# Kernel optimization log

Hardware: AMD Instinct MI355X
Metric: run time of the kernel (lower is better)

## Reference

```python
import jax, jax.numpy as jnp
import numpy as np
import math

NUM_HEADS = 16
KEY_DIM = 64
MODEL_DIM = 1024
NEG_INF = -1000000000.0


def _get_slopes(n):
    def pow2_slopes(n):
        start = 2 ** (-2 ** (-(math.log2(n) - 3)))
        return [start * start ** i for i in range(n)]
    if math.log2(n).is_integer():
        s = pow2_slopes(n)
    else:
        c = 2 ** math.floor(math.log2(n))
        s = pow2_slopes(c) + pow2_slopes(2 * c)[0::2][: n - c]
    return jnp.asarray(s, dtype=jnp.float32)


def setup_inputs() -> dict:
    key = jax.random.key(0)
    ks = jax.random.split(key, 11)
    B, S, D = 4, 2048, MODEL_DIM
    P = NUM_HEADS * KEY_DIM
    sd = 1.0 / math.sqrt(D)
    return {
        "query": jax.random.normal(ks[0], (B, S, D), jnp.float32),
        "key": jax.random.normal(ks[1], (B, S, D), jnp.float32),
        "value": jax.random.normal(ks[2], (B, S, D), jnp.float32),
        "Wq": jax.random.normal(ks[3], (D, P), jnp.float32) * sd,
        "bq": jnp.zeros((P,), jnp.float32),
        "Wk": jax.random.normal(ks[4], (D, P), jnp.float32) * sd,
        "bk": jnp.zeros((P,), jnp.float32),
        "Wv": jax.random.normal(ks[5], (D, P), jnp.float32) * sd,
        "bv": jnp.zeros((P,), jnp.float32),
        "Wo": jax.random.normal(ks[6], (P, D), jnp.float32) * (1.0 / math.sqrt(P)),
        "bo": jnp.zeros((D,), jnp.float32),
    }


def reference(query, key, value, Wq, bq, Wk, bk, Wv, bv, Wo, bo):
    B, S, _ = query.shape
    H, Kd = NUM_HEADS, KEY_DIM

    def split_heads(x):  # [B,S,H*Kd] -> [B,H,S,Kd]
        return x.reshape(B, S, H, Kd).transpose(0, 2, 1, 3)

    q = split_heads(query @ Wq + bq)
    k = split_heads(key @ Wk + bk)
    v = split_heads(value @ Wv + bv)

    logits = jnp.einsum("bhqd,bhkd->bhqk", q, k) / jnp.sqrt(jnp.float32(Kd))

    i = jnp.arange(S)[:, None]
    j = jnp.arange(S)[None, :]
    causal = jnp.where(i >= j, 0.0, NEG_INF).astype(jnp.float32)  # [S,S]
    rel = (i - j).astype(jnp.float32)  # [S,S]
    slopes = _get_slopes(H)  # [H]
    alibi = slopes[:, None, None] * rel  # [H,S,S]
    logits = logits + causal[None, None, :, :] + alibi[None, :, :, :]

    weights = jax.nn.softmax(logits, axis=-1)
    attn = jnp.einsum("bhqk,bhkd->bhqd", weights, v)
    concat = attn.transpose(0, 2, 1, 3).reshape(B, S, H * Kd)
    return concat @ Wo + bo
```

## Files before the change

### kernel.cpp

```cpp
#include <hip/hip_runtime.h>

#define B_ 4
#define S_ 2048
#define D_ 1024
#define H_ 16
#define KD_ 64
#define P_ 1024
#define M_ (B_*S_)

typedef unsigned short u16;
typedef unsigned int u32;
typedef __attribute__((ext_vector_type(4))) float f32x4;
typedef __attribute__((ext_vector_type(8))) __bf16 bf16x8;

__device__ __forceinline__ u16 f2bf(float f) {
  u32 x = __float_as_uint(f);
  return (u16)((x + 0x7fffu + ((x >> 16) & 1u)) >> 16);
}

__device__ __forceinline__ void gl_lds16(const u16* g, u16* l) {
  __builtin_amdgcn_global_load_lds((__attribute__((address_space(1))) void*)g,
                                   (__attribute__((address_space(3))) void*)l, 16, 0, 0);
}

__device__ __forceinline__ u32 pkbf(float a, float b) {
  return __builtin_amdgcn_perm(__float_as_uint(b) + 0x8000u,
                               __float_as_uint(a) + 0x8000u, 0x07060302u);
}

__global__ void cvt3_kernel(const float* __restrict__ q, const float* __restrict__ k,
                            const float* __restrict__ v,
                            u16* __restrict__ Xq, u16* __restrict__ Xk, u16* __restrict__ Xv) {
  const int z = blockIdx.y;
  const float* in = z == 0 ? q : z == 1 ? k : v;
  u16* out = z == 0 ? Xq : z == 1 ? Xk : Xv;
  int i = blockIdx.x * 256 + threadIdx.x;
  float4 vv = ((const float4*)in)[i];
  ((u32*)out)[i*2+0] = (u32)f2bf(vv.x) | ((u32)f2bf(vv.y) << 16);
  ((u32*)out)[i*2+1] = (u32)f2bf(vv.z) | ((u32)f2bf(vv.w) << 16);
}

__global__ void transpose_cvt4(const float* __restrict__ Wq, const float* __restrict__ Wk,
                               const float* __restrict__ Wv, const float* __restrict__ Wo,
                               u16* __restrict__ WqT, u16* __restrict__ WkT,
                               u16* __restrict__ WvT, u16* __restrict__ WoT) {
  const int z = blockIdx.z;
  const float* in = z == 0 ? Wq : z == 1 ? Wk : z == 2 ? Wv : Wo;
  u16* out = z == 0 ? WqT : z == 1 ? WkT : z == 2 ? WvT : WoT;
  __shared__ float tile[32][33];
  int bx = blockIdx.x * 32, by = blockIdx.y * 32;
  int tx = threadIdx.x, ty = threadIdx.y;
  #pragma unroll
  for (int kk = 0; kk < 4; ++kk)
    tile[ty + kk*8][tx] = in[(by + ty + kk*8) * 1024 + bx + tx];
  __syncthreads();
  #pragma unroll
  for (int kk = 0; kk < 4; ++kk)
    out[(bx + ty + kk*8) * 1024 + by + tx] = f2bf(tile[tx][ty + kk*8]);
}

__global__ __launch_bounds__(256) void gemm_qkv(
    const u16* __restrict__ Xq, const u16* __restrict__ Xk, const u16* __restrict__ Xv,
    const u16* __restrict__ WqT, const u16* __restrict__ WkT, const u16* __restrict__ WvT,
    const float* __restrict__ bq, const float* __restrict__ bk, const float* __restrict__ bv,
    u16* __restrict__ Qb, u16* __restrict__ Kb, u16* __restrict__ Vt)
{
  constexpr int K = 1024, N = 1024, BK = 32;
  const int z = blockIdx.z;
  const u16* A  = z == 0 ? Xq  : z == 1 ? Xk  : Xv;
  const u16* Bt = z == 0 ? WqT : z == 1 ? WkT : WvT;
  const float* bias = z == 0 ? bq : z == 1 ? bk : bv;

  __shared__ alignas(16) u16 As[128*BK];
  __shared__ alignas(16) u16 Bs[128*BK];
  const int tid = threadIdx.x;
  const int w = tid >> 6, l = tid & 63;
  const int quad = l >> 4, l16 = l & 15;
  const int wm = (w >> 1) * 64, wn = (w & 1) * 64;
  const long mBase = (long)blockIdx.x * 128;
  const int  nBase = blockIdx.y * 128;

  f32x4 acc[4][4] = {};
  const int off0 = w*1024 + l*16;

  for (int kb = 0; kb < K/BK; ++kb) {
    __syncthreads();
    #pragma unroll
    for (int p = 0; p < 2; ++p) {
      int off = p*4096 + off0;
      int row = off >> 6;
      int cb  = off & 63;
      const u16* ga = A  + (mBase + row)*K + kb*BK + (cb >> 1);
      const u16* gb = Bt + ((long)(nBase + row))*K + kb*BK + (cb >> 1);
      gl_lds16(ga, (u16*)((char*)As + p*4096 + w*1024));
      gl_lds16(gb, (u16*)((char*)Bs + p*4096 + w*1024));
    }
    __syncthreads();
    bf16x8 af[4], bf[4];
    #pragma unroll
    for (int i = 0; i < 4; ++i) af[i] = *(const bf16x8*)&As[(wm + i*16 + l16)*BK + quad*8];
    #pragma unroll
    for (int j = 0; j < 4; ++j) bf[j] = *(const bf16x8*)&Bs[(wn + j*16 + l16)*BK + quad*8];
    #pragma unroll
    for (int i = 0; i < 4; ++i)
      #pragma unroll
      for (int j = 0; j < 4; ++j)
        acc[i][j] = __builtin_amdgcn_mfma_f32_16x16x32_bf16(af[i], bf[j], acc[i][j], 0, 0, 0);
  }

  if (z < 2) {
    u16* Cout = z == 0 ? Qb : Kb;
    #pragma unroll
    for (int i = 0; i < 4; ++i)
      #pragma unroll
      for (int j = 0; j < 4; ++j)
        #pragma unroll
        for (int r = 0; r < 4; ++r) {
          long row = mBase + wm + i*16 + quad*4 + r;
          int  col = nBase + wn + j*16 + l16;
          Cout[row*N + col] = f2bf(acc[i][j][r] + bias[col]);
        }
  } else {
    #pragma unroll
    for (int i = 0; i < 4; ++i)
      #pragma unroll
      for (int j = 0; j < 4; ++j) {
        int  col  = nBase + wn + j*16 + l16;
        long row0 = mBase + wm + i*16 + quad*4;
        int  bb = (int)(row0 >> 11);
        int  ss = (int)(row0 & 2047);
        float bcol = bias[col];
        float v0 = acc[i][j][0] + bcol, v1 = acc[i][j][1] + bcol;
        float v2 = acc[i][j][2] + bcol, v3 = acc[i][j][3] + bcol;
        uint2 pk;
        pk.x = (u32)f2bf(v0) | ((u32)f2bf(v1) << 16);
        pk.y = (u32)f2bf(v2) | ((u32)f2bf(v3) << 16);
        *(uint2*)&Vt[((long)(bb*16) * 64 + col) * 2048 + ss] = pk;
      }
  }
}

__global__ __launch_bounds__(256) void gemm_out(const u16* __restrict__ A,
                                                const u16* __restrict__ Bt,
                                                const float* __restrict__ bias,
                                                float* __restrict__ Cout)
{
  constexpr int K = 1024, N = 1024, BK = 32;
  __shared__ alignas(16) u16 As[128*BK];
  __shared__ alignas(16) u16 Bs[128*BK];
  const int tid = threadIdx.x;
  const int w = tid >> 6, l = tid & 63;
  const int quad = l >> 4, l16 = l & 15;
  const int wm = (w >> 1) * 64, wn = (w & 1) * 64;
  const long mBase = (long)blockIdx.x * 128;
  const int  nBase = blockIdx.y * 128;

  f32x4 acc[4][4] = {};
  const int off0 = w*1024 + l*16;

  for (int kb = 0; kb < K/BK; ++kb) {
    __syncthreads();
    #pragma unroll
    for (int p = 0; p < 2; ++p) {
      int off = p*4096 + off0;
      int row = off >> 6;
      int cb  = off & 63;
      const u16* ga = A  + (mBase + row)*K + kb*BK + (cb >> 1);
      const u16* gb = Bt + ((long)(nBase + row))*K + kb*BK + (cb >> 1);
      gl_lds16(ga, (u16*)((char*)As + p*4096 + w*1024));
      gl_lds16(gb, (u16*)((char*)Bs + p*4096 + w*1024));
    }
    __syncthreads();
    bf16x8 af[4], bf[4];
    #pragma unroll
    for (int i = 0; i < 4; ++i) af[i] = *(const bf16x8*)&As[(wm + i*16 + l16)*BK + quad*8];
    #pragma unroll
    for (int j = 0; j < 4; ++j) bf[j] = *(const bf16x8*)&Bs[(wn + j*16 + l16)*BK + quad*8];
    #pragma unroll
    for (int i = 0; i < 4; ++i)
      #pragma unroll
      for (int j = 0; j < 4; ++j)
        acc[i][j] = __builtin_amdgcn_mfma_f32_16x16x32_bf16(af[i], bf[j], acc[i][j], 0, 0, 0);
  }

  #pragma unroll
  for (int i = 0; i < 4; ++i)
    #pragma unroll
    for (int j = 0; j < 4; ++j)
      #pragma unroll
      for (int r = 0; r < 4; ++r) {
        long row = mBase + wm + i*16 + quad*4 + r;
        int  col = nBase + wn + j*16 + l16;
        Cout[row*N + col] = acc[i][j][r] + bias[col];
      }
}

#define PST 136
__global__ __launch_bounds__(64, 3) void attn_kernel(const u16* __restrict__ Qb,
                                                     const u16* __restrict__ Kb,
                                                     const u16* __restrict__ Vt,
                                                     u16* __restrict__ Ob)
{
  const int n = blockIdx.x;
  const int qt = 15 - (n >> 8);
  const int r8 = n & 255;
  const int b = r8 >> 6, h = (r8 >> 2) & 15, w = r8 & 3;
  const int l = threadIdx.x;
  const int quad = l >> 4, l16 = l & 15;
  const float LOG2E = 1.44269504089f;
  const float slope = exp2f(-0.5f * (float)(h + 1));
  const float c1  = 0.125f * LOG2E;
  const float sl2 = slope * LOG2E;

  __shared__ alignas(16) u16 Ps[2][16][PST];

  const int q0 = qt*128 + w*32;
  const u16* Qp = Qb + ((long)(b*S_ + q0))*P_ + h*KD_;
  const u16* Kp = Kb + ((long)(b*S_))*P_ + h*KD_;
  const u16* Vp = Vt + ((long)(b*H_ + h))*KD_*S_;

  bf16x8 qf[2][2];
  #pragma unroll
  for (int i = 0; i < 2; ++i)
    #pragma unroll
    for (int kk = 0; kk < 2; ++kk)
      qf[i][kk] = *(const bf16x8*)&Qp[(long)(i*16 + l16)*P_ + kk*32 + quad*8];

  f32x4 o[2][4] = {};
  float lsum[2] = {0.f, 0.f};
  const float rs1 = sl2, rs2 = 2.f*sl2, rs3 = 3.f*sl2;

  for (int kt = 0; kt < qt; ++kt) {
    const u16* kts = Kp + (long)(kt*128 + l16)*P_;
    #pragma unroll
    for (int jh = 0; jh < 2; ++jh) {
      f32x4 st[2][4];
      #pragma unroll
      for (int jj = 0; jj < 4; ++jj) {
        const int j = jh*4 + jj;
        const u16* kp = kts + (long)(j*16)*P_;
        bf16x8 kf0 = *(const bf16x8*)(kp + quad*8);
        bf16x8 kf1 = *(const bf16x8*)(kp + 32 + quad*8);
        #pragma unroll
        for (int i = 0; i < 2; ++i) {
          f32x4 t = {};
          t = __builtin_amdgcn_mfma_f32_16x16x32_bf16(kf0, qf[i][0], t, 0, 0, 0);
          t = __builtin_amdgcn_mfma_f32_16x16x32_bf16(kf1, qf[i][1], t, 0, 0, 0);
          st[i][jj] = t;
        }
      }
      #pragma unroll
      for (int i = 0; i < 2; ++i)
        #pragma unroll
        for (int jj = 0; jj < 4; ++jj) {
          const int j = jh*4 + jj;
          const float kb  = (float)(kt*128 + j*16 + quad*4);
          const float bij = -sl2 * kb;
          float p0 = __builtin_amdgcn_exp2f(fmaf(st[i][jj][0], c1, bij));
          float p1 = __builtin_amdgcn_exp2f(fmaf(st[i][jj][1], c1, bij) - rs1);
          float p2 = __builtin_amdgcn_exp2f(fmaf(st[i][jj][2], c1, bij) - rs2);
          float p3 = __builtin_amdgcn_exp2f(fmaf(st[i][jj][3], c1, bij) - rs3);
          lsum[i] += (p0 + p1) + (p2 + p3);
          uint2 pk; pk.x = pkbf(p0, p1); pk.y = pkbf(p2, p3);
          *(uint2*)&Ps[i][l16][j*16 + quad*4] = pk;
        }
    }
    #pragma unroll
    for (int ks = 0; ks < 4; ++ks) {
      bf16x8 pb0 = *(const bf16x8*)&Ps[0][l16][ks*32 + quad*8];
      bf16x8 pb1 = *(const bf16x8*)&Ps[1][l16][ks*32 + quad*8];
      #pragma unroll
      for (int jn = 0; jn < 4; ++jn) {
        bf16x8 vf = *(const bf16x8*)&Vp[(long)(jn*16 + l16)*S_ + kt*128 + ks*32 + quad*8];
        o[0][jn] = __builtin_amdgcn_mfma_f32_16x16x32_bf16(vf, pb0, o[0][jn], 0, 0, 0);
        o[1][jn] = __builtin_amdgcn_mfma_f32_16x16x32_bf16(vf, pb1, o[1][jn], 0, 0, 0);
      }
    }
  }

  {
    const int kt = qt;
    const int jmax = 2*w + 2, ksmax = w + 1;
    const u16* kts = Kp + (long)(kt*128 + l16)*P_;
    for (int j = 0; j < jmax; ++j) {
      const u16* kp = kts + (long)(j*16)*P_;
      bf16x8 kf0 = *(const bf16x8*)(kp + quad*8);
      bf16x8 kf1 = *(const bf16x8*)(kp + 32 + quad*8);
      const int kl0 = j*16 + quad*4;
      const float kb  = (float)(kt*128 + kl0);
      #pragma unroll
      for (int i = 0; i < 2; ++i) {
        f32x4 t = {};
        t = __builtin_amdgcn_mfma_f32_16x16x32_bf16(kf0, qf[i][0], t, 0, 0, 0);
        t = __builtin_amdgcn_mfma_f32_16x16x32_bf16(kf1, qf[i][1], t, 0, 0, 0);
        const int ql = w*32 + i*16 + l16;
        const float bij = -sl2 * kb;
        float x0 = fmaf(t[0], c1, bij);
        float x1 = fmaf(t[1], c1, bij) - rs1;
        float x2 = fmaf(t[2], c1, bij) - rs2;
        float x3 = fmaf(t[3], c1, bij) - rs3;
        if (kl0 + 0 > ql) x0 = -1e30f;
        if (kl0 + 1 > ql) x1 = -1e30f;
        if (kl0 + 2 > ql) x2 = -1e30f;
        if (kl0 + 3 > ql) x3 = -1e30f;
        float p0 = __builtin_amdgcn_exp2f(x0);
        float p1 = __builtin_amdgcn_exp2f(x1);
        float p2 = __builtin_amdgcn_exp2f(x2);
        float p3 = __builtin_amdgcn_exp2f(x3);
        lsum[i] += (p0 + p1) + (p2 + p3);
        uint2 pk; pk.x = pkbf(p0, p1); pk.y = pkbf(p2, p3);
        *(uint2*)&Ps[i][l16][j*16 + quad*4] = pk;
      }
    }
    for (int ks = 0; ks < ksmax; ++ks) {
      bf16x8 pb0 = *(const bf16x8*)&Ps[0][l16][ks*32 + quad*8];
      bf16x8 pb1 = *(const bf16x8*)&Ps[1][l16][ks*32 + quad*8];
      #pragma unroll
      for (int jn = 0; jn < 4; ++jn) {
        bf16x8 vf = *(const bf16x8*)&Vp[(long)(jn*16 + l16)*S_ + kt*128 + ks*32 + quad*8];
        o[0][jn] = __builtin_amdgcn_mfma_f32_16x16x32_bf16(vf, pb0, o[0][jn], 0, 0, 0);
        o[1][jn] = __builtin_amdgcn_mfma_f32_16x16x32_bf16(vf, pb1, o[1][jn], 0, 0, 0);
      }
    }
  }

  #pragma unroll
  for (int i = 0; i < 2; ++i) {
    lsum[i] += __shfl_xor(lsum[i], 16, 64);
    lsum[i] += __shfl_xor(lsum[i], 32, 64);
    const float inv = 1.0f / lsum[i];
    #pragma unroll
    for (int jn = 0; jn < 4; ++jn) {
      float v0 = o[i][jn][0] * inv, v1 = o[i][jn][1] * inv;
      float v2 = o[i][jn][2] * inv, v3 = o[i][jn][3] * inv;
      uint2 pk;
      pk.x = (u32)f2bf(v0) | ((u32)f2bf(v1) << 16);
      pk.y = (u32)f2bf(v2) | ((u32)f2bf(v3) << 16);
      *(uint2*)&Ob[((long)(b*S_ + q0 + i*16 + l16))*P_ + h*KD_ + jn*16 + quad*4] = pk;
    }
  }
}

extern "C" void kernel_launch(void* const* d_in, const int* in_sizes, int n_in,
                              void* d_out, int out_size, void* d_ws, size_t ws_size,
                              hipStream_t stream) {
  const float* q  = (const float*)d_in[0];
  const float* k  = (const float*)d_in[1];
  const float* v  = (const float*)d_in[2];
  const float* Wq = (const float*)d_in[3];
  const float* bq = (const float*)d_in[4];
  const float* Wk = (const float*)d_in[5];
  const float* bk = (const float*)d_in[6];
  const float* Wv = (const float*)d_in[7];
  const float* bv = (const float*)d_in[8];
  const float* Wo = (const float*)d_in[9];
  const float* bo = (const float*)d_in[10];

  const size_t X_ELEMS = (size_t)M_ * P_;
  const size_t W_ELEMS = (size_t)D_ * P_;
  u16* ws  = (u16*)d_ws;
  u16* Xq  = ws;
  u16* Xk  = Xq  + X_ELEMS;
  u16* Xv  = Xk  + X_ELEMS;
  u16* WqT = Xv  + X_ELEMS;
  u16* WkT = WqT + W_ELEMS;
  u16* WvT = WkT + W_ELEMS;
  u16* WoT = WvT + W_ELEMS;
  u16* Qb  = WoT + W_ELEMS;
  u16* Kb  = Qb  + X_ELEMS;
  u16* Vt  = Kb  + X_ELEMS;
  u16* Attn = Xq;

  cvt3_kernel<<<dim3((unsigned)(X_ELEMS/4/256), 3), 256, 0, stream>>>(q, k, v, Xq, Xk, Xv);

  transpose_cvt4<<<dim3(32, 32, 4), dim3(32, 8), 0, stream>>>(Wq, Wk, Wv, Wo,
                                                              WqT, WkT, WvT, WoT);

  gemm_qkv<<<dim3(M_/128, P_/128, 3), 256, 0, stream>>>(Xq, Xk, Xv, WqT, WkT, WvT,
                                                        bq, bk, bv, Qb, Kb, Vt);

  attn_kernel<<<dim3(4096), 64, 0, stream>>>(Qb, Kb, Vt, Attn);

  gemm_out<<<dim3(M_/128, P_/128), 256, 0, stream>>>(Attn, WoT, bo, (float*)d_out);
}
```

Measured before the change: 402.8 us.

## Keep attention probabilities in registers via permlane swaps instead of LDS

The attention kernel now gives each wave 16 query rows instead of 32 and launches 256-thread blocks of four waves. The softmax probability tiles are no longer staged through shared memory. They are rearranged into the MFMA B-operand layout in registers using permlane32/16 swaps, with a ds_bpermute fallback. This removes the LDS round trip and cuts register pressure, allowing more waves per CU. The cost is that each K and V fragment is loaded by twice as many waves, which doubles global and L2 traffic per query row.

```diff
diff --git a/kernel.cpp b/kernel.cpp
--- a/kernel.cpp
+++ b/kernel.cpp
@@ -10,6 +10,7 @@
 
 typedef unsigned short u16;
 typedef unsigned int u32;
+typedef __attribute__((ext_vector_type(2))) unsigned u32x2;
 typedef __attribute__((ext_vector_type(4))) float f32x4;
 typedef __attribute__((ext_vector_type(8))) __bf16 bf16x8;
 
@@ -27,6 +28,28 @@
   return __builtin_amdgcn_perm(__float_as_uint(b) + 0x8000u,
                                __float_as_uint(a) + 0x8000u, 0x07060302u);
 }
+
+#if __has_builtin(__builtin_amdgcn_permlane32_swap) && __has_builtin(__builtin_amdgcn_permlane16_swap)
+__device__ __forceinline__ void plswap(u32& a, u32& b) {
+  u32x2 r32 = __builtin_amdgcn_permlane32_swap(a, b, false, false);
+  u32x2 r16 = __builtin_amdgcn_permlane16_swap(r32[0], r32[1], false, false);
+  a = r16[0]; b = r16[1];
+}
+#else
+__device__ __forceinline__ void plswap(u32& a, u32& b) {
+  const int l = threadIdx.x & 63;
+  const int quad = l >> 4, l16 = l & 15;
+  int i0 = (((quad & 1) * 32) + l16) * 4;
+  int i1 = i0 + 64;
+  int a_lo = __builtin_amdgcn_ds_bpermute(i0, (int)a);
+  int b_lo = __builtin_amdgcn_ds_bpermute(i0, (int)b);
+  int a_hi = __builtin_amdgcn_ds_bpermute(i1, (int)a);
+  int b_hi = __builtin_amdgcn_ds_bpermute(i1, (int)b);
+  u32 na = (quad < 2) ? (u32)a_lo : (u32)b_lo;
+  u32 nb = (quad < 2) ? (u32)a_hi : (u32)b_hi;
+  a = na; b = nb;
+}
+#endif
 
 __global__ void cvt3_kernel(const float* __restrict__ q, const float* __restrict__ k,
                             const float* __restrict__ v,
@@ -195,149 +218,142 @@
       }
 }
 
-#define PST 136
-__global__ __launch_bounds__(64, 3) void attn_kernel(const u16* __restrict__ Qb,
-                                                     const u16* __restrict__ Kb,
-                                                     const u16* __restrict__ Vt,
-                                                     u16* __restrict__ Ob)
+__global__ __launch_bounds__(256, 8) void attn_kernel(const u16* __restrict__ Qb,
+                                                      const u16* __restrict__ Kb,
+                                                      const u16* __restrict__ Vt,
+                                                      u16* __restrict__ Ob)
 {
   const int n = blockIdx.x;
-  const int qt = 15 - (n >> 8);
-  const int r8 = n & 255;
-  const int b = r8 >> 6, h = (r8 >> 2) & 15, w = r8 & 3;
-  const int l = threadIdx.x;
+  const int qt = 15 - (n >> 7);
+  const int r7 = n & 127;
+  const int bh = r7 >> 1;
+  const int b = bh >> 4, h = bh & 15;
+  const int sw = (r7 & 1) * 4 + (threadIdx.x >> 6);
+  const int l = threadIdx.x & 63;
   const int quad = l >> 4, l16 = l & 15;
   const float LOG2E = 1.44269504089f;
   const float slope = exp2f(-0.5f * (float)(h + 1));
   const float c1  = 0.125f * LOG2E;
   const float sl2 = slope * LOG2E;
-
-  __shared__ alignas(16) u16 Ps[2][16][PST];
-
-  const int q0 = qt*128 + w*32;
+  const float rs1 = sl2, rs2 = 2.f*sl2, rs3 = 3.f*sl2;
+
+  const int q0 = qt*128 + sw*16;
   const u16* Qp = Qb + ((long)(b*S_ + q0))*P_ + h*KD_;
   const u16* Kp = Kb + ((long)(b*S_))*P_ + h*KD_;
   const u16* Vp = Vt + ((long)(b*H_ + h))*KD_*S_;
 
-  bf16x8 qf[2][2];
+  bf16x8 qf[2];
   #pragma unroll
-  for (int i = 0; i < 2; ++i)
-    #pragma unroll
-    for (int kk = 0; kk < 2; ++kk)
-      qf[i][kk] = *(const bf16x8*)&Qp[(long)(i*16 + l16)*P_ + kk*32 + quad*8];
-
-  f32x4 o[2][4] = {};
-  float lsum[2] = {0.f, 0.f};
-  const float rs1 = sl2, rs2 = 2.f*sl2, rs3 = 3.f*sl2;
+  for (int kk = 0; kk < 2; ++kk)
+    qf[kk] = *(const bf16x8*)&Qp[(long)l16*P_ + kk*32 + quad*8];
+
+  f32x4 o[4] = {};
+  float lsum = 0.f;
 
   for (int kt = 0; kt < qt; ++kt) {
     const u16* kts = Kp + (long)(kt*128 + l16)*P_;
-    #pragma unroll
-    for (int jh = 0; jh < 2; ++jh) {
-      f32x4 st[2][4];
-      #pragma unroll
-      for (int jj = 0; jj < 4; ++jj) {
-        const int j = jh*4 + jj;
+    const float kbase = (float)(kt*128);
+    #pragma unroll
+    for (int ks = 0; ks < 4; ++ks) {
+      u32 pw[2][2];
+      #pragma unroll
+      for (int jp = 0; jp < 2; ++jp) {
+        const int j = 2*ks + jp;
         const u16* kp = kts + (long)(j*16)*P_;
         bf16x8 kf0 = *(const bf16x8*)(kp + quad*8);
         bf16x8 kf1 = *(const bf16x8*)(kp + 32 + quad*8);
-        #pragma unroll
-        for (int i = 0; i < 2; ++i) {
-          f32x4 t = {};
-          t = __builtin_amdgcn_mfma_f32_16x16x32_bf16(kf0, qf[i][0], t, 0, 0, 0);
-          t = __builtin_amdgcn_mfma_f32_16x16x32_bf16(kf1, qf[i][1], t, 0, 0, 0);
-          st[i][jj] = t;
-        }
-      }
-      #pragma unroll
-      for (int i = 0; i < 2; ++i)
-        #pragma unroll
-        for (int jj = 0; jj < 4; ++jj) {
-          const int j = jh*4 + jj;
-          const float kb  = (float)(kt*128 + j*16 + quad*4);
-          const float bij = -sl2 * kb;
-          float p0 = __builtin_amdgcn_exp2f(fmaf(st[i][jj][0], c1, bij));
-          float p1 = __builtin_amdgcn_exp2f(fmaf(st[i][jj][1], c1, bij) - rs1);
-          float p2 = __builtin_amdgcn_exp2f(fmaf(st[i][jj][2], c1, bij) - rs2);
-          float p3 = __builtin_amdgcn_exp2f(fmaf(st[i][jj][3], c1, bij) - rs3);
-          lsum[i] += (p0 + p1) + (p2 + p3);
-          uint2 pk; pk.x = pkbf(p0, p1); pk.y = pkbf(p2, p3);
-          *(uint2*)&Ps[i][l16][j*16 + quad*4] = pk;
-        }
-    }
-    #pragma unroll
-    for (int ks = 0; ks < 4; ++ks) {
-      bf16x8 pb0 = *(const bf16x8*)&Ps[0][l16][ks*32 + quad*8];
-      bf16x8 pb1 = *(const bf16x8*)&Ps[1][l16][ks*32 + quad*8];
+        f32x4 t = {};
+        t = __builtin_amdgcn_mfma_f32_16x16x32_bf16(kf0, qf[0], t, 0, 0, 0);
+        t = __builtin_amdgcn_mfma_f32_16x16x32_bf16(kf1, qf[1], t, 0, 0, 0);
+        const float bij = -sl2 * (kbase + (float)(j*16 + quad*4));
+        float p0 = __builtin_amdgcn_exp2f(fmaf(t[0], c1, bij));
+        float p1 = __builtin_amdgcn_exp2f(fmaf(t[1], c1, bij) - rs1);
+        float p2 = __builtin_amdgcn_exp2f(fmaf(t[2], c1, bij) - rs2);
+        float p3 = __builtin_amdgcn_exp2f(fmaf(t[3], c1, bij) - rs3);
+        lsum += (p0 + p1) + (p2 + p3);
+        pw[jp][0] = pkbf(p0, p1);
+        pw[jp][1] = pkbf(p2, p3);
+      }
+      u32 fa0 = pw[0][0], fb0 = pw[1][0];
+      u32 fa1 = pw[0][1], fb1 = pw[1][1];
+      plswap(fa0, fb0);
+      plswap(fa1, fb1);
+      union { u32 u[4]; bf16x8 v; } fu;
+      fu.u[0] = fa0; fu.u[1] = fa1; fu.u[2] = fb0; fu.u[3] = fb1;
+      const bf16x8 pb = fu.v;
       #pragma unroll
       for (int jn = 0; jn < 4; ++jn) {
         bf16x8 vf = *(const bf16x8*)&Vp[(long)(jn*16 + l16)*S_ + kt*128 + ks*32 + quad*8];
-        o[0][jn] = __builtin_amdgcn_mfma_f32_16x16x32_bf16(vf, pb0, o[0][jn], 0, 0, 0);
-        o[1][jn] = __builtin_amdgcn_mfma_f32_16x16x32_bf16(vf, pb1, o[1][jn], 0, 0, 0);
+        o[jn] = __builtin_amdgcn_mfma_f32_16x16x32_bf16(vf, pb, o[jn], 0, 0, 0);
       }
     }
   }
 
   {
     const int kt = qt;
-    const int jmax = 2*w + 2, ksmax = w + 1;
+    const int ksmax = (sw >> 1) + 1;
     const u16* kts = Kp + (long)(kt*128 + l16)*P_;
-    for (int j = 0; j < jmax; ++j) {
-      const u16* kp = kts + (long)(j*16)*P_;
-      bf16x8 kf0 = *(const bf16x8*)(kp + quad*8);
-      bf16x8 kf1 = *(const bf16x8*)(kp + 32 + quad*8);
-      const int kl0 = j*16 + quad*4;
-      const float kb  = (float)(kt*128 + kl0);
-      #pragma unroll
-      for (int i = 0; i < 2; ++i) {
-        f32x4 t = {};
-        t = __builtin_amdgcn_mfma_f32_16x16x32_bf16(kf0, qf[i][0], t, 0, 0, 0);
-        t = __builtin_amdgcn_mfma_f32_16x16x32_bf16(kf1, qf[i][1], t, 0, 0, 0);
-        const int ql = w*32 + i*16 + l16;
-        const float bij = -sl2 * kb;
-        float x0 = fmaf(t[0], c1, bij);
-        float x1 = fmaf(t[1], c1, bij) - rs1;
-        float x2 = fmaf(t[2], c1, bij) - rs2;
-        float x3 = fmaf(t[3], c1, bij) - rs3;
-        if (kl0 + 0 > ql) x0 = -1e30f;
-        if (kl0 + 1 > ql) x1 = -1e30f;
-        if (kl0 + 2 > ql) x2 = -1e30f;
-        if (kl0 + 3 > ql) x3 = -1e30f;
-        float p0 = __builtin_amdgcn_exp2f(x0);
-        float p1 = __builtin_amdgcn_exp2f(x1);
-        float p2 = __builtin_amdgcn_exp2f(x2);
-        float p3 = __builtin_amdgcn_exp2f(x3);
-        lsum[i] += (p0 + p1) + (p2 + p3);
-        uint2 pk; pk.x = pkbf(p0, p1); pk.y = pkbf(p2, p3);
-        *(uint2*)&Ps[i][l16][j*16 + quad*4] = pk;
-      }
-    }
+    const int ql = sw*16 + l16;
     for (int ks = 0; ks < ksmax; ++ks) {
-      bf16x8 pb0 = *(const bf16x8*)&Ps[0][l16][ks*32 + quad*8];
-      bf16x8 pb1 = *(const bf16x8*)&Ps[1][l16][ks*32 + quad*8];
+      u32 pw[2][2];
+      #pragma unroll
+      for (int jp = 0; jp < 2; ++jp) {
+        const int j = 2*ks + jp;
+        if (j <= sw) {
+          const u16* kp = kts + (long)(j*16)*P_;
+          bf16x8 kf0 = *(const bf16x8*)(kp + quad*8);
+          bf16x8 kf1 = *(const bf16x8*)(kp + 32 + quad*8);
+          f32x4 t = {};
+          t = __builtin_amdgcn_mfma_f32_16x16x32_bf16(kf0, qf[0], t, 0, 0, 0);
+          t = __builtin_amdgcn_mfma_f32_16x16x32_bf16(kf1, qf[1], t, 0, 0, 0);
+          const int kl0 = j*16 + quad*4;
+          const float bij = -sl2 * (float)(kt*128 + kl0);
+          float x0 = fmaf(t[0], c1, bij);
+          float x1 = fmaf(t[1], c1, bij) - rs1;
+          float x2 = fmaf(t[2], c1, bij) - rs2;
+          float x3 = fmaf(t[3], c1, bij) - rs3;
+          if (kl0 + 0 > ql) x0 = -1e30f;
+          if (kl0 + 1 > ql) x1 = -1e30f;
+          if (kl0 + 2 > ql) x2 = -1e30f;
+          if (kl0 + 3 > ql) x3 = -1e30f;
+          float p0 = __builtin_amdgcn_exp2f(x0);
+          float p1 = __builtin_amdgcn_exp2f(x1);
+          float p2 = __builtin_amdgcn_exp2f(x2);
+          float p3 = __builtin_amdgcn_exp2f(x3);
+          lsum += (p0 + p1) + (p2 + p3);
+          pw[jp][0] = pkbf(p0, p1);
+          pw[jp][1] = pkbf(p2, p3);
+        } else {
+          pw[jp][0] = 0u;
+          pw[jp][1] = 0u;
+        }
+      }
+      u32 fa0 = pw[0][0], fb0 = pw[1][0];
+      u32 fa1 = pw[0][1], fb1 = pw[1][1];
+      plswap(fa0, fb0);
+      plswap(fa1, fb1);
+      union { u32 u[4]; bf16x8 v; } fu;
+      fu.u[0] = fa0; fu.u[1] = fa1; fu.u[2] = fb0; fu.u[3] = fb1;
+      const bf16x8 pb = fu.v;
       #pragma unroll
       for (int jn = 0; jn < 4; ++jn) {
         bf16x8 vf = *(const bf16x8*)&Vp[(long)(jn*16 + l16)*S_ + kt*128 + ks*32 + quad*8];
-        o[0][jn] = __builtin_amdgcn_mfma_f32_16x16x32_bf16(vf, pb0, o[0][jn], 0, 0, 0);
-        o[1][jn] = __builtin_amdgcn_mfma_f32_16x16x32_bf16(vf, pb1, o[1][jn], 0, 0, 0);
+        o[jn] = __builtin_amdgcn_mfma_f32_16x16x32_bf16(vf, pb, o[jn], 0, 0, 0);
       }
     }
   }
 
+  lsum += __shfl_xor(lsum, 16, 64);
+  lsum += __shfl_xor(lsum, 32, 64);
+  const float inv = 1.0f / lsum;
   #pragma unroll
-  for (int i = 0; i < 2; ++i) {
-    lsum[i] += __shfl_xor(lsum[i], 16, 64);
-    lsum[i] += __shfl_xor(lsum[i], 32, 64);
-    const float inv = 1.0f / lsum[i];
-    #pragma unroll
-    for (int jn = 0; jn < 4; ++jn) {
-      float v0 = o[i][jn][0] * inv, v1 = o[i][jn][1] * inv;
-      float v2 = o[i][jn][2] * inv, v3 = o[i][jn][3] * inv;
-      uint2 pk;
-      pk.x = (u32)f2bf(v0) | ((u32)f2bf(v1) << 16);
-      pk.y = (u32)f2bf(v2) | ((u32)f2bf(v3) << 16);
-      *(uint2*)&Ob[((long)(b*S_ + q0 + i*16 + l16))*P_ + h*KD_ + jn*16 + quad*4] = pk;
-    }
+  for (int jn = 0; jn < 4; ++jn) {
+    float v0 = o[jn][0] * inv, v1 = o[jn][1] * inv;
+    float v2 = o[jn][2] * inv, v3 = o[jn][3] * inv;
+    uint2 pk;
+    pk.x = (u32)f2bf(v0) | ((u32)f2bf(v1) << 16);
+    pk.y = (u32)f2bf(v2) | ((u32)f2bf(v3) << 16);
+    *(uint2*)&Ob[((long)(b*S_ + q0 + l16))*P_ + h*KD_ + jn*16 + quad*4] = pk;
   }
 }
 
@@ -379,7 +395,7 @@
   gemm_qkv<<<dim3(M_/128, P_/128, 3), 256, 0, stream>>>(Xq, Xk, Xv, WqT, WkT, WvT,
                                                         bq, bk, bv, Qb, Kb, Vt);
 
-  attn_kernel<<<dim3(4096), 64, 0, stream>>>(Qb, Kb, Vt, Attn);
+  attn_kernel<<<dim3(2048), 256, 0, stream>>>(Qb, Kb, Vt, Attn);
 
   gemm_out<<<dim3(M_/128, P_/128), 256, 0, stream>>>(Attn, WoT, bo, (float*)d_out);
 }
```

Measured after the change: 565.8 us. 1.4x slower.

## Keep softmax P tile in registers via permlane swaps instead of LDS round-trip

Applied to the files above, without the earlier changes.

The attention kernel no longer writes the bf16 probability tile to shared memory and reads it back as the B operand of the PV MFMA. Instead, each 32-key slice is computed and then rearranged across lanes with permlane32/permlane16 swaps (with a ds_bpermute fallback) so it matches the MFMA operand layout. Score and PV computation are now interleaved per 32-key slice. This removes the LDS traffic and its wait latency, in exchange for extra cross-lane instructions and a different schedule.

```diff
diff --git a/kernel.cpp b/kernel.cpp
--- a/kernel.cpp
+++ b/kernel.cpp
@@ -10,6 +10,7 @@
 
 typedef unsigned short u16;
 typedef unsigned int u32;
+typedef __attribute__((ext_vector_type(2))) unsigned u32x2;
 typedef __attribute__((ext_vector_type(4))) float f32x4;
 typedef __attribute__((ext_vector_type(8))) __bf16 bf16x8;
 
@@ -27,6 +28,28 @@
   return __builtin_amdgcn_perm(__float_as_uint(b) + 0x8000u,
                                __float_as_uint(a) + 0x8000u, 0x07060302u);
 }
+
+#if __has_builtin(__builtin_amdgcn_permlane32_swap) && __has_builtin(__builtin_amdgcn_permlane16_swap)
+__device__ __forceinline__ void plswap(u32& a, u32& b) {
+  u32x2 r32 = __builtin_amdgcn_permlane32_swap(a, b, false, false);
+  u32x2 r16 = __builtin_amdgcn_permlane16_swap(r32[0], r32[1], false, false);
+  a = r16[0]; b = r16[1];
+}
+#else
+__device__ __forceinline__ void plswap(u32& a, u32& b) {
+  const int l = threadIdx.x & 63;
+  const int quad = l >> 4, l16 = l & 15;
+  int i0 = (((quad & 1) * 32) + l16) * 4;
+  int i1 = i0 + 64;
+  int a_lo = __builtin_amdgcn_ds_bpermute(i0, (int)a);
+  int b_lo = __builtin_amdgcn_ds_bpermute(i0, (int)b);
+  int a_hi = __builtin_amdgcn_ds_bpermute(i1, (int)a);
+  int b_hi = __builtin_amdgcn_ds_bpermute(i1, (int)b);
+  u32 na = (quad < 2) ? (u32)a_lo : (u32)b_lo;
+  u32 nb = (quad < 2) ? (u32)a_hi : (u32)b_hi;
+  a = na; b = nb;
+}
+#endif
 
 __global__ void cvt3_kernel(const float* __restrict__ q, const float* __restrict__ k,
                             const float* __restrict__ v,
@@ -195,7 +218,6 @@
       }
 }
 
-#define PST 136
 __global__ __launch_bounds__(64, 3) void attn_kernel(const u16* __restrict__ Qb,
                                                      const u16* __restrict__ Kb,
                                                      const u16* __restrict__ Vt,
@@ -211,8 +233,7 @@
   const float slope = exp2f(-0.5f * (float)(h + 1));
   const float c1  = 0.125f * LOG2E;
   const float sl2 = slope * LOG2E;
-
-  __shared__ alignas(16) u16 Ps[2][16][PST];
+  const float rs1 = sl2, rs2 = 2.f*sl2, rs3 = 3.f*sl2;
 
   const int q0 = qt*128 + w*32;
   const u16* Qp = Qb + ((long)(b*S_ + q0))*P_ + h*KD_;
@@ -228,98 +249,107 @@
 
   f32x4 o[2][4] = {};
   float lsum[2] = {0.f, 0.f};
-  const float rs1 = sl2, rs2 = 2.f*sl2, rs3 = 3.f*sl2;
 
   for (int kt = 0; kt < qt; ++kt) {
     const u16* kts = Kp + (long)(kt*128 + l16)*P_;
-    #pragma unroll
-    for (int jh = 0; jh < 2; ++jh) {
-      f32x4 st[2][4];
-      #pragma unroll
-      for (int jj = 0; jj < 4; ++jj) {
-        const int j = jh*4 + jj;
+    const float kbase = (float)(kt*128);
+    #pragma unroll
+    for (int ks = 0; ks < 4; ++ks) {
+      u32 pw[2][2][2];
+      #pragma unroll
+      for (int jp = 0; jp < 2; ++jp) {
+        const int j = 2*ks + jp;
         const u16* kp = kts + (long)(j*16)*P_;
         bf16x8 kf0 = *(const bf16x8*)(kp + quad*8);
         bf16x8 kf1 = *(const bf16x8*)(kp + 32 + quad*8);
+        const float bij = -sl2 * (kbase + (float)(j*16 + quad*4));
         #pragma unroll
         for (int i = 0; i < 2; ++i) {
           f32x4 t = {};
           t = __builtin_amdgcn_mfma_f32_16x16x32_bf16(kf0, qf[i][0], t, 0, 0, 0);
           t = __builtin_amdgcn_mfma_f32_16x16x32_bf16(kf1, qf[i][1], t, 0, 0, 0);
-          st[i][jj] = t;
+          float p0 = __builtin_amdgcn_exp2f(fmaf(t[0], c1, bij));
+          float p1 = __builtin_amdgcn_exp2f(fmaf(t[1], c1, bij) - rs1);
+          float p2 = __builtin_amdgcn_exp2f(fmaf(t[2], c1, bij) - rs2);
+          float p3 = __builtin_amdgcn_exp2f(fmaf(t[3], c1, bij) - rs3);
+          lsum[i] += (p0 + p1) + (p2 + p3);
+          pw[i][jp][0] = pkbf(p0, p1);
+          pw[i][jp][1] = pkbf(p2, p3);
         }
       }
-      #pragma unroll
-      for (int i = 0; i < 2; ++i)
-        #pragma unroll
-        for (int jj = 0; jj < 4; ++jj) {
-          const int j = jh*4 + jj;
-          const float kb  = (float)(kt*128 + j*16 + quad*4);
-          const float bij = -sl2 * kb;
-          float p0 = __builtin_amdgcn_exp2f(fmaf(st[i][jj][0], c1, bij));
-          float p1 = __builtin_amdgcn_exp2f(fmaf(st[i][jj][1], c1, bij) - rs1);
-          float p2 = __builtin_amdgcn_exp2f(fmaf(st[i][jj][2], c1, bij) - rs2);
-          float p3 = __builtin_amdgcn_exp2f(fmaf(st[i][jj][3], c1, bij) - rs3);
-          lsum[i] += (p0 + p1) + (p2 + p3);
-          uint2 pk; pk.x = pkbf(p0, p1); pk.y = pkbf(p2, p3);
-          *(uint2*)&Ps[i][l16][j*16 + quad*4] = pk;
-        }
-    }
-    #pragma unroll
-    for (int ks = 0; ks < 4; ++ks) {
-      bf16x8 pb0 = *(const bf16x8*)&Ps[0][l16][ks*32 + quad*8];
-      bf16x8 pb1 = *(const bf16x8*)&Ps[1][l16][ks*32 + quad*8];
+      bf16x8 pb[2];
+      #pragma unroll
+      for (int i = 0; i < 2; ++i) {
+        u32 fa0 = pw[i][0][0], fb0 = pw[i][1][0];
+        u32 fa1 = pw[i][0][1], fb1 = pw[i][1][1];
+        plswap(fa0, fb0);
+        plswap(fa1, fb1);
+        union { u32 u[4]; bf16x8 v; } fu;
+        fu.u[0] = fa0; fu.u[1] = fa1; fu.u[2] = fb0; fu.u[3] = fb1;
+        pb[i] = fu.v;
+      }
       #pragma unroll
       for (int jn = 0; jn < 4; ++jn) {
         bf16x8 vf = *(const bf16x8*)&Vp[(long)(jn*16 + l16)*S_ + kt*128 + ks*32 + quad*8];
-        o[0][jn] = __builtin_amdgcn_mfma_f32_16x16x32_bf16(vf, pb0, o[0][jn], 0, 0, 0);
-        o[1][jn] = __builtin_amdgcn_mfma_f32_16x16x32_bf16(vf, pb1, o[1][jn], 0, 0, 0);
+        o[0][jn] = __builtin_amdgcn_mfma_f32_16x16x32_bf16(vf, pb[0], o[0][jn], 0, 0, 0);
+        o[1][jn] = __builtin_amdgcn_mfma_f32_16x16x32_bf16(vf, pb[1], o[1][jn], 0, 0, 0);
       }
     }
   }
 
   {
     const int kt = qt;
-    const int jmax = 2*w + 2, ksmax = w + 1;
+    const int ksmax = w + 1;
     const u16* kts = Kp + (long)(kt*128 + l16)*P_;
-    for (int j = 0; j < jmax; ++j) {
-      const u16* kp = kts + (long)(j*16)*P_;
-      bf16x8 kf0 = *(const bf16x8*)(kp + quad*8);
-      bf16x8 kf1 = *(const bf16x8*)(kp + 32 + quad*8);
-      const int kl0 = j*16 + quad*4;
-      const float kb  = (float)(kt*128 + kl0);
+    for (int ks = 0; ks < ksmax; ++ks) {
+      u32 pw[2][2][2];
+      #pragma unroll
+      for (int jp = 0; jp < 2; ++jp) {
+        const int j = 2*ks + jp;
+        const u16* kp = kts + (long)(j*16)*P_;
+        bf16x8 kf0 = *(const bf16x8*)(kp + quad*8);
+        bf16x8 kf1 = *(const bf16x8*)(kp + 32 + quad*8);
+        const int kl0 = j*16 + quad*4;
+        const float bij = -sl2 * (float)(kt*128 + kl0);
+        #pragma unroll
+        for (int i = 0; i < 2; ++i) {
+          const int ql = w*32 + i*16 + l16;
+          f32x4 t = {};
+          t = __builtin_amdgcn_mfma_f32_16x16x32_bf16(kf0, qf[i][0], t, 0, 0, 0);
+          t = __builtin_amdgcn_mfma_f32_16x16x32_bf16(kf1, qf[i][1], t, 0, 0, 0);
+          float x0 = fmaf(t[0], c1, bij);
+          float x1 = fmaf(t[1], c1, bij) - rs1;
+          float x2 = fmaf(t[2], c1, bij) - rs2;
+          float x3 = fmaf(t[3], c1, bij) - rs3;
+          if (kl0 + 0 > ql) x0 = -1e30f;
+          if (kl0 + 1 > ql) x1 = -1e30f;
+          if (kl0 + 2 > ql) x2 = -1e30f;
+          if (kl0 + 3 > ql) x3 = -1e30f;
+          float p0 = __builtin_amdgcn_exp2f(x0);
+          float p1 = __builtin_amdgcn_exp2f(x1);
+          float p2 = __builtin_amdgcn_exp2f(x2);
+          float p3 = __builtin_amdgcn_exp2f(x3);
+          lsum[i] += (p0 + p1) + (p2 + p3);
+          pw[i][jp][0] = pkbf(p0, p1);
+          pw[i][jp][1] = pkbf(p2, p3);
+        }
+      }
+      bf16x8 pb[2];
       #pragma unroll
       for (int i = 0; i < 2; ++i) {
-        f32x4 t = {};
-        t = __builtin_amdgcn_mfma_f32_16x16x32_bf16(kf0, qf[i][0], t, 0, 0, 0);
-        t = __builtin_amdgcn_mfma_f32_16x16x32_bf16(kf1, qf[i][1], t, 0, 0, 0);
-        const int ql = w*32 + i*16 + l16;
-        const float bij = -sl2 * kb;
-        float x0 = fmaf(t[0], c1, bij);
-        float x1 = fmaf(t[1], c1, bij) - rs1;
-        float x2 = fmaf(t[2], c1, bij) - rs2;
-        float x3 = fmaf(t[3], c1, bij) - rs3;
-        if (kl0 + 0 > ql) x0 = -1e30f;
-        if (kl0 + 1 > ql) x1 = -1e30f;
-        if (kl0 + 2 > ql) x2 = -1e30f;
-        if (kl0 + 3 > ql) x3 = -1e30f;
-        float p0 = __builtin_amdgcn_exp2f(x0);
-        float p1 = __builtin_amdgcn_exp2f(x1);
-        float p2 = __builtin_amdgcn_exp2f(x2);
-        float p3 = __builtin_amdgcn_exp2f(x3);
-        lsum[i] += (p0 + p1) + (p2 + p3);
-        uint2 pk; pk.x = pkbf(p0, p1); pk.y = pkbf(p2, p3);
-        *(uint2*)&Ps[i][l16][j*16 + quad*4] = pk;
-      }
-    }
-    for (int ks = 0; ks < ksmax; ++ks) {
-      bf16x8 pb0 = *(const bf16x8*)&Ps[0][l16][ks*32 + quad*8];
-      bf16x8 pb1 = *(const bf16x8*)&Ps[1][l16][ks*32 + quad*8];
+        u32 fa0 = pw[i][0][0], fb0 = pw[i][1][0];
+        u32 fa1 = pw[i][0][1], fb1 = pw[i][1][1];
+        plswap(fa0, fb0);
+        plswap(fa1, fb1);
+        union { u32 u[4]; bf16x8 v; } fu;
+        fu.u[0] = fa0; fu.u[1] = fa1; fu.u[2] = fb0; fu.u[3] = fb1;
+        pb[i] = fu.v;
+      }
       #pragma unroll
       for (int jn = 0; jn < 4; ++jn) {
         bf16x8 vf = *(const bf16x8*)&Vp[(long)(jn*16 + l16)*S_ + kt*128 + ks*32 + quad*8];
-        o[0][jn] = __builtin_amdgcn_mfma_f32_16x16x32_bf16(vf, pb0, o[0][jn], 0, 0, 0);
-        o[1][jn] = __builtin_amdgcn_mfma_f32_16x16x32_bf16(vf, pb1, o[1][jn], 0, 0, 0);
+        o[0][jn] = __builtin_amdgcn_mfma_f32_16x16x32_bf16(vf, pb[0], o[0][jn], 0, 0, 0);
+        o[1][jn] = __builtin_amdgcn_mfma_f32_16x16x32_bf16(vf, pb[1], o[1][jn], 0, 0, 0);
       }
     }
   }
```

Result: no change. 398.3 us (-1.1%).
